# Kernel optimization log

Measured on AMD Instinct MI355X. Metric: run time of the kernel, lower is better.

The kernel has to match this reference:

```python
import jax, jax.numpy as jnp
import numpy as np


def setup_inputs() -> dict:
    key = jax.random.key(0)
    k1, k2 = jax.random.split(key)
    B, T, D = 32, 512, 384
    x = jax.random.normal(k1, (B, T, D), dtype=jnp.float32)
    duration = jax.random.randint(k2, (B, T), 0, 8, dtype=jnp.int32)
    max_length = 4096  # T * max_duration, worst-case expanded mel length
    return {"x": x, "duration": duration, "max_length": max_length}


def reference(x, duration, max_length):
    # x: [B, T, D] float; duration: [B, T] int; returns padded expanded
    # sequence [B, M, D] and mel positions [B, M] (1-based, 0 for padding).
    B, T, D = x.shape
    cum = jnp.cumsum(duration, axis=1)          # [B, T] cumulative frame offsets
    total = cum[:, -1]                          # [B] total mel frames per batch
    frames = jnp.arange(max_length)             # [M]
    # For output frame j, source token = first i with cum[i] > j
    tok = jax.vmap(lambda c: jnp.searchsorted(c, frames, side='right'))(cum)  # [B, M]
    tok = jnp.clip(tok, 0, T - 1)
    valid = frames[None, :] < total[:, None]    # [B, M]
    out = jnp.take_along_axis(x, tok[:, :, None], axis=1)   # [B, M, D]
    out = out * valid[:, :, None].astype(x.dtype)            # zero-pad tail
    mel_pos = jnp.where(valid, frames[None, :] + 1, 0)       # [B, M]
    return out, mel_pos
```

## Files before the change

kernel.cpp:

```cpp
#include <hip/hip_runtime.h>


constexpr int B  = 32;
constexpr int T  = 512;
constexpr int D  = 384;
constexpr int ML = 4096;
constexpr int D4 = D / 4;
constexpr int FPB = 128;
constexpr int BLOCKS_PER_BATCH = ML / FPB;
constexpr int NT = 256;

__global__ __launch_bounds__(NT) void lr_kernel(
        const float4* __restrict__ x,
        const int*    __restrict__ dur,
        float*        __restrict__ outf,
        float*        __restrict__ mel)
{
    __shared__ int s_cum[T];
    __shared__ int s_tok[FPB];
    __shared__ int s_part[NT];

    const int b      = blockIdx.x / BLOCKS_PER_BATCH;
    const int fchunk = blockIdx.x % BLOCKS_PER_BATCH;
    const int f0     = fchunk * FPB;
    const int tid    = threadIdx.x;

    const int d0 = dur[b * T + 2 * tid];
    const int d1 = dur[b * T + 2 * tid + 1];
    const int pair = d0 + d1;
    s_part[tid] = pair;
    __syncthreads();
    int val = pair;
    #pragma unroll
    for (int off = 1; off < NT; off <<= 1) {
        int t = (tid >= off) ? s_part[tid - off] : 0;
        __syncthreads();
        val += t;
        s_part[tid] = val;
        __syncthreads();
    }
    const int excl = val - pair;
    s_cum[2 * tid]     = excl + d0;
    s_cum[2 * tid + 1] = excl + pair;
    __syncthreads();
    const int total = s_cum[T - 1];

    if (tid < FPB) {
        const int f = f0 + tid;
        int lo = 0, hi = T;
        while (lo < hi) {
            const int mid = (lo + hi) >> 1;
            if (s_cum[mid] <= f) lo = mid + 1; else hi = mid;
        }
        const int tok = (lo < T - 1) ? lo : (T - 1);
        s_tok[tid] = (f < total) ? tok : -1;
        mel[b * ML + f] = (f < total) ? (float)(f + 1) : 0.0f;
    }
    __syncthreads();

    float4* __restrict__ out4 = (float4*)outf;
    const float4 zero4 = make_float4(0.f, 0.f, 0.f, 0.f);
    const size_t out_base = ((size_t)b * ML + f0) * D4;
    const size_t x_base   = (size_t)b * T * D4;
    #pragma unroll 4
    for (int i = tid; i < FPB * D4; i += NT) {
        const int lf  = i / D4;
        const int c   = i - lf * D4;
        const int tok = s_tok[lf];
        float4 v = zero4;
        if (tok >= 0) v = x[x_base + (size_t)tok * D4 + c];
        out4[out_base + (size_t)lf * D4 + c] = v;
    }
}

extern "C" void kernel_launch(void* const* d_in, const int* in_sizes, int n_in,
                              void* d_out, int out_size, void* d_ws, size_t ws_size,
                              hipStream_t stream) {
    const float4* x   = (const float4*)d_in[0];
    const int*    dur = (const int*)d_in[1];
    float* outf = (float*)d_out;
    float* mel  = outf + (size_t)B * ML * D;

    dim3 grid(B * BLOCKS_PER_BATCH);
    dim3 block(NT);
    lr_kernel<<<grid, block, 0, stream>>>(x, dur, outf, mel);
}
```

Before: 231.7 us.

## Split token lookup into separate kernel; add XCD-aware mapping and nontemporal stores

Token indices are now computed once per batch in a small pre-kernel that writes short tokens to workspace. Before, every copy block redid the 512-element scan and binary search. The copy kernel remaps block IDs so each XCD handles four contiguous batches, which keeps x rows in that XCD's L2. It also uses nontemporal stores for the large output, takes a fast path for fully padded or fully valid chunks, and adds a second launch plus a workspace round-trip.

```diff
diff --git a/kernel.cpp b/kernel.cpp
--- a/kernel.cpp
+++ b/kernel.cpp
@@ -1,14 +1,120 @@
 #include <hip/hip_runtime.h>
 
 
-constexpr int B  = 32;
-constexpr int T  = 512;
-constexpr int D  = 384;
-constexpr int ML = 4096;
-constexpr int D4 = D / 4;
+constexpr int B   = 32;
+constexpr int T   = 512;
+constexpr int D   = 384;
+constexpr int ML  = 4096;
+constexpr int D4  = D / 4;
+constexpr int NT  = 256;
 constexpr int FPB = 128;
 constexpr int BLOCKS_PER_BATCH = ML / FPB;
-constexpr int NT = 256;
+constexpr int NXCD = 8;
+
+typedef float f32x4 __attribute__((ext_vector_type(4)));
+
+__global__ __launch_bounds__(NT) void tok_kernel(
+        const int* __restrict__ dur,
+        short*     __restrict__ tok)
+{
+    __shared__ int s_cum[T];
+    __shared__ int s_part[NT];
+
+    const int blk = blockIdx.x;
+    const int xcd = blk & (NXCD - 1);
+    const int j   = blk >> 3;
+    const int b   = xcd * 4 + (j >> 3);
+    const int seg = j & 7;
+    const int tid = threadIdx.x;
+
+    const int d0 = dur[b * T + 2 * tid];
+    const int d1 = dur[b * T + 2 * tid + 1];
+    const int pair = d0 + d1;
+    s_part[tid] = pair;
+    __syncthreads();
+    int val = pair;
+    #pragma unroll
+    for (int off = 1; off < NT; off <<= 1) {
+        int t = (tid >= off) ? s_part[tid - off] : 0;
+        __syncthreads();
+        val += t;
+        s_part[tid] = val;
+        __syncthreads();
+    }
+    const int excl = val - pair;
+    s_cum[2 * tid]     = excl + d0;
+    s_cum[2 * tid + 1] = excl + pair;
+    __syncthreads();
+    const int total = s_cum[T - 1];
+
+    #pragma unroll
+    for (int k = 0; k < 2; ++k) {
+        const int f = seg * 512 + k * NT + tid;
+        int lo = 0, hi = T;
+        while (lo < hi) {
+            const int mid = (lo + hi) >> 1;
+            if (s_cum[mid] <= f) lo = mid + 1; else hi = mid;
+        }
+        const int tk = (lo < T - 1) ? lo : (T - 1);
+        tok[b * ML + f] = (f < total) ? (short)tk : (short)-1;
+    }
+}
+
+__global__ __launch_bounds__(NT) void copy_kernel(
+        const f32x4*  __restrict__ x,
+        const short*  __restrict__ tok,
+        f32x4*        __restrict__ out4,
+        float*        __restrict__ mel)
+{
+    __shared__ short s_tok[FPB];
+
+    const int blk = blockIdx.x;
+    const int xcd = blk & (NXCD - 1);
+    const int j   = blk >> 3;
+    const int b   = xcd * 4 + (j >> 5);
+    const int fchunk = j & 31;
+    const int f0  = fchunk * FPB;
+    const int tid = threadIdx.x;
+
+    if (tid < FPB) {
+        const short tk = tok[b * ML + f0 + tid];
+        s_tok[tid] = tk;
+        const float mv = (tk >= 0) ? (float)(f0 + tid + 1) : 0.0f;
+        __builtin_nontemporal_store(mv, &mel[b * ML + f0 + tid]);
+    }
+    __syncthreads();
+
+    const size_t out_base = ((size_t)b * ML + f0) * D4;
+    const f32x4 zero4 = {0.f, 0.f, 0.f, 0.f};
+
+    if (s_tok[0] < 0) {
+        #pragma unroll 8
+        for (int i = tid; i < FPB * D4; i += NT)
+            __builtin_nontemporal_store(zero4, &out4[out_base + i]);
+        return;
+    }
+
+    const size_t x_base = (size_t)b * T * D4;
+    if (s_tok[FPB - 1] >= 0) {
+        #pragma unroll 4
+        for (int i = tid; i < FPB * D4; i += NT) {
+            const int lf = i / D4;
+            const int c  = i - lf * D4;
+            const f32x4 v = x[x_base + (size_t)s_tok[lf] * D4 + c];
+            __builtin_nontemporal_store(v, &out4[out_base + i]);
+        }
+    } else {
+        #pragma unroll 4
+        for (int i = tid; i < FPB * D4; i += NT) {
+            const int lf = i / D4;
+            const int c  = i - lf * D4;
+            const int tk = s_tok[lf];
+            f32x4 v = zero4;
+            if (tk >= 0) v = x[x_base + (size_t)tk * D4 + c];
+            __builtin_nontemporal_store(v, &out4[out_base + i]);
+        }
+    }
+}
 
 __global__ __launch_bounds__(NT) void lr_kernel(
         const float4* __restrict__ x,
@@ -76,12 +182,19 @@
 extern "C" void kernel_launch(void* const* d_in, const int* in_sizes, int n_in,
                               void* d_out, int out_size, void* d_ws, size_t ws_size,
                               hipStream_t stream) {
-    const float4* x   = (const float4*)d_in[0];
+    const float*  xf  = (const float*)d_in[0];
     const int*    dur = (const int*)d_in[1];
     float* outf = (float*)d_out;
     float* mel  = outf + (size_t)B * ML * D;
 
-    dim3 grid(B * BLOCKS_PER_BATCH);
-    dim3 block(NT);
-    lr_kernel<<<grid, block, 0, stream>>>(x, dur, outf, mel);
-}
+    const size_t tok_bytes = (size_t)B * ML * sizeof(short);
+    if (d_ws != nullptr && ws_size >= tok_bytes) {
+        short* tok = (short*)d_ws;
+        tok_kernel<<<dim3(256), dim3(NT), 0, stream>>>(dur, tok);
+        copy_kernel<<<dim3(B * BLOCKS_PER_BATCH), dim3(NT), 0, stream>>>(
+            (const f32x4*)xf, tok, (f32x4*)outf, mel);
+    } else {
+        lr_kernel<<<dim3(B * BLOCKS_PER_BATCH), dim3(NT), 0, stream>>>(
+            (const float4*)xf, dur, outf, mel);
+    }
+}
```

New measurement: 245.3 us. 5.9% more time.

## Use nontemporal stores, fast paths for padded chunks, smaller frame chunks

Applied to the files above, without the earlier changes.

Halves frames per block so there are twice as many blocks, and writes all outputs with nontemporal stores so the large output stream bypasses cache retention. Blocks that lie entirely in the padding region only write zeros and skip reading x. Fully valid blocks skip the per-element validity check. The copy loop is restructured so each warp-sized group of 32 lanes copies rows with fixed column offsets, removing the per-element division. Halving the chunk doubles the prefix-sum work, which every block repeats.

```diff
diff --git a/kernel.cpp b/kernel.cpp
--- a/kernel.cpp
+++ b/kernel.cpp
@@ -1,27 +1,31 @@
 #include <hip/hip_runtime.h>
 
 
-constexpr int B  = 32;
-constexpr int T  = 512;
-constexpr int D  = 384;
-constexpr int ML = 4096;
-constexpr int D4 = D / 4;
-constexpr int FPB = 128;
-constexpr int BLOCKS_PER_BATCH = ML / FPB;
-constexpr int NT = 256;
+constexpr int B   = 32;
+constexpr int T   = 512;
+constexpr int D   = 384;
+constexpr int ML  = 4096;
+constexpr int D4  = D / 4;
+constexpr int NT  = 256;
+constexpr int FPB = 64;
+constexpr int CHUNKS = ML / FPB;
+constexpr int NVEC = FPB * D4;
+
+typedef float f32x4 __attribute__((ext_vector_type(4)));
 
 __global__ __launch_bounds__(NT) void lr_kernel(
-        const float4* __restrict__ x,
-        const int*    __restrict__ dur,
-        float*        __restrict__ outf,
-        float*        __restrict__ mel)
+        const f32x4* __restrict__ x,
+        const int*   __restrict__ dur,
+        f32x4*       __restrict__ out4,
+        float*       __restrict__ mel)
 {
-    __shared__ int s_cum[T];
-    __shared__ int s_tok[FPB];
-    __shared__ int s_part[NT];
+    __shared__ int   s_cum[T];
+    __shared__ int   s_part[NT];
+    __shared__ short s_tok[FPB];
 
-    const int b      = blockIdx.x / BLOCKS_PER_BATCH;
-    const int fchunk = blockIdx.x % BLOCKS_PER_BATCH;
+    const int blk    = blockIdx.x;
+    const int b      = blk >> 6;
+    const int fchunk = blk & (CHUNKS - 1);
     const int f0     = fchunk * FPB;
     const int tid    = threadIdx.x;
 
@@ -52,36 +56,74 @@
             const int mid = (lo + hi) >> 1;
             if (s_cum[mid] <= f) lo = mid + 1; else hi = mid;
         }
-        const int tok = (lo < T - 1) ? lo : (T - 1);
-        s_tok[tid] = (f < total) ? tok : -1;
-        mel[b * ML + f] = (f < total) ? (float)(f + 1) : 0.0f;
+        const int tk = (lo < T - 1) ? lo : (T - 1);
+        s_tok[tid] = (f < total) ? (short)tk : (short)-1;
+        const float mv = (f < total) ? (float)(f + 1) : 0.0f;
+        __builtin_nontemporal_store(mv, &mel[b * ML + f]);
     }
     __syncthreads();
 
-    float4* __restrict__ out4 = (float4*)outf;
-    const float4 zero4 = make_float4(0.f, 0.f, 0.f, 0.f);
     const size_t out_base = ((size_t)b * ML + f0) * D4;
-    const size_t x_base   = (size_t)b * T * D4;
-    #pragma unroll 4
-    for (int i = tid; i < FPB * D4; i += NT) {
-        const int lf  = i / D4;
-        const int c   = i - lf * D4;
-        const int tok = s_tok[lf];
-        float4 v = zero4;
-        if (tok >= 0) v = x[x_base + (size_t)tok * D4 + c];
-        out4[out_base + (size_t)lf * D4 + c] = v;
+    const f32x4  zero4    = {0.f, 0.f, 0.f, 0.f};
+
+    if (s_tok[FPB - 1] < 0) {
+        if (s_tok[0] < 0) {
+            #pragma unroll
+            for (int i = tid; i < NVEC; i += NT)
+                __builtin_nontemporal_store(zero4, &out4[out_base + i]);
+            return;
+        }
+        const size_t x_base = (size_t)b * T * D4;
+        const int c2 = tid & 31;
+        const int fg = tid >> 5;
+        #pragma unroll
+        for (int k = 0; k < FPB / 8; ++k) {
+            const int lf = fg + (k << 3);
+            const int tk = s_tok[lf];
+            const size_t orow = out_base + (size_t)lf * D4;
+            if (tk >= 0) {
+                const size_t xrow = x_base + (size_t)tk * D4;
+                #pragma unroll
+                for (int j = 0; j < 3; ++j) {
+                    const int c = c2 + (j << 5);
+                    __builtin_nontemporal_store(x[xrow + c], &out4[orow + c]);
+                }
+            } else {
+                #pragma unroll
+                for (int j = 0; j < 3; ++j)
+                    __builtin_nontemporal_store(zero4, &out4[orow + c2 + (j << 5)]);
+            }
+        }
+        return;
+    }
+
+    {
+        const size_t x_base = (size_t)b * T * D4;
+        const int c2 = tid & 31;
+        const int fg = tid >> 5;
+        #pragma unroll
+        for (int k = 0; k < FPB / 8; ++k) {
+            const int lf = fg + (k << 3);
+            const size_t xrow = x_base + (size_t)s_tok[lf] * D4;
+            const size_t orow = out_base + (size_t)lf * D4;
+            #pragma unroll
+            for (int j = 0; j < 3; ++j) {
+                const int c = c2 + (j << 5);
+                __builtin_nontemporal_store(x[xrow + c], &out4[orow + c]);
+            }
+        }
     }
 }
 
 extern "C" void kernel_launch(void* const* d_in, const int* in_sizes, int n_in,
                               void* d_out, int out_size, void* d_ws, size_t ws_size,
                               hipStream_t stream) {
-    const float4* x   = (const float4*)d_in[0];
-    const int*    dur = (const int*)d_in[1];
+    const f32x4* x   = (const f32x4*)d_in[0];
+    const int*   dur = (const int*)d_in[1];
     float* outf = (float*)d_out;
     float* mel  = outf + (size_t)B * ML * D;
 
-    dim3 grid(B * BLOCKS_PER_BATCH);
+    dim3 grid(B * CHUNKS);
     dim3 block(NT);
-    lr_kernel<<<grid, block, 0, stream>>>(x, dur, outf, mel);
+    lr_kernel<<<grid, block, 0, stream>>>(x, dur, (f32x4*)outf, mel);
 }
```

New measurement: 229.7 us. About the same (-0.9%).
